# Kernel tuning notes

Hardware: AMD Instinct MI355X
Metric: run time of the kernel (lower is better)

The kernel has to match this reference:

```python
import jax, jax.numpy as jnp
import numpy as np

T, N, XD, H, Z, E = 6, 4096, 64, 256, 128, 131072


def setup_inputs() -> dict:
    key = jax.random.key(0)
    ks = jax.random.split(key, 16)
    f32 = jnp.float32
    def rn(k, shp):
        return jax.random.normal(k, shp, f32)
    def gl(k, shp):  # glorot-ish init, scaled by fan_in
        return jax.random.normal(k, shp, f32) * np.float32(1.0 / np.sqrt(shp[-2]))
    return {
        "x": rn(ks[0], (T, N, XD)),
        "edges": jax.random.randint(ks[1], (T, 2, E), 0, N, dtype=jnp.int32),
        "eps": rn(ks[2], (T, N, Z)),
        "drop_u": jax.random.uniform(ks[3], (T, N, Z), f32),
        "phi_x_w": gl(ks[4], (XD, H)), "phi_x_b": jnp.zeros((H,), f32),
        "phi_z_w": gl(ks[5], (Z, H)), "phi_z_b": jnp.zeros((H,), f32),
        "enc_w": gl(ks[6], (2 * H, H)),
        "enc_mu_w": gl(ks[7], (H, Z)),
        "enc_lv_w": gl(ks[8], (H, Z)),
        "prior_w": gl(ks[9], (H, H)), "prior_b": jnp.zeros((H,), f32),
        "prior_mu_w": gl(ks[10], (H, Z)), "prior_mu_b": jnp.zeros((Z,), f32),
        "prior_lv_w": gl(ks[11], (H, Z)), "prior_lv_b": jnp.zeros((Z,), f32),
        "gru_wx": gl(ks[12], (4, 2 * H, H)),  # gates i,f,o,c; x-side GCN weights
        "gru_wh": gl(ks[13], (4, H, H)),      # gates i,f,o,c; h-side GCN weights
    }


def reference(x, edges, eps, drop_u, phi_x_w, phi_x_b, phi_z_w, phi_z_b,
              enc_w, enc_mu_w, enc_lv_w, prior_w, prior_b,
              prior_mu_w, prior_mu_b, prior_lv_w, prior_lv_b,
              gru_wx, gru_wh):
    T_, N_, _ = x.shape
    H_ = phi_x_w.shape[1]
    h = jnp.zeros((N_, H_), x.dtype)
    c = jnp.zeros((N_, H_), x.dtype)
    loop = jnp.arange(N_, dtype=edges.dtype)
    enc_mus, prior_mus = [], []
    dec_t = None
    for t in range(T_):  # fixed small T; edge structure differs per step
        row = jnp.concatenate([edges[t, 0], loop])  # add self loops
        col = jnp.concatenate([edges[t, 1], loop])
        deg = jax.ops.segment_sum(jnp.ones(row.shape, x.dtype), row, num_segments=N_)
        dinv = jnp.where(deg > 0, jax.lax.rsqrt(deg), jnp.zeros((), x.dtype))
        norm = (dinv[row] * dinv[col])[:, None]

        def gcn(xx, W):
            # GCNConv: xW, gather at col, scale by sym-norm, scatter-add at row
            return jax.ops.segment_sum(norm * (xx @ W)[col], row, num_segments=N_)

        phi_x_t = jax.nn.relu(x[t] @ phi_x_w + phi_x_b)
        enc_t = jax.nn.relu(gcn(jnp.concatenate([phi_x_t, h], axis=1), enc_w))
        enc_mu_t = gcn(enc_t, enc_mu_w)
        enc_std_t = jax.nn.softplus(gcn(enc_t, enc_lv_w))
        prior_t = jax.nn.relu(h @ prior_w + prior_b)
        prior_mu_t = prior_t @ prior_mu_w + prior_mu_b
        _prior_std_t = jax.nn.softplus(prior_t @ prior_lv_w + prior_lv_b)  # computed as in original, unused in returns
        z_t = eps[t] * enc_std_t + enc_mu_t  # original: eps.mul(logvar).add_(mu)
        phi_z_t = jax.nn.relu(z_t @ phi_z_w + phi_z_b)
        # InnerProductDecoder with dropout(p=0.5, training=True), identity act
        z_drop = jnp.where(drop_u[t] < 0.5, z_t * 2.0, jnp.zeros((), x.dtype))
        dec_t = z_drop @ z_drop.T  # [N, N]
        # graph-LSTM step (n_layer = 1)
        xin = jnp.concatenate([phi_x_t, phi_z_t], axis=1)  # [N, 2H]
        gi = jax.nn.sigmoid(gcn(xin, gru_wx[0]) + gcn(h, gru_wh[0]))
        gf = jax.nn.sigmoid(gcn(xin, gru_wx[1]) + gcn(h, gru_wh[1]))
        go = jax.nn.sigmoid(gcn(xin, gru_wx[2]) + gcn(h, gru_wh[2]))
        ct = jnp.tanh(gcn(xin, gru_wx[3]) + gcn(h, gru_wh[3]))
        c_new = gf * h + gi * ct    # faithful to original: F_g * h[i] (not c)
        h_new = go * jnp.tanh(c)    # faithful to original: uses old c[i]
        h, c = h_new, c_new
        enc_mus.append(enc_mu_t)
        prior_mus.append(prior_mu_t)
    return jnp.stack(enc_mus), jnp.stack(prior_mus), h[None], dec_t
```

## Files before the change

kernel.cpp:

```cpp
#include <hip/hip_runtime.h>
#include <hip/hip_bf16.h>
#include <math.h>

#define T_  6
#define NN  4096
#define XD_ 64
#define H_  256
#define ZZ  128
#define EE  131072

typedef unsigned short u16;
typedef __attribute__((ext_vector_type(8))) short short8;
typedef __attribute__((ext_vector_type(8))) unsigned short u16x8;
typedef __attribute__((ext_vector_type(4))) float f32x4;

__device__ __forceinline__ float bf2f(u16 u) { return __uint_as_float(((unsigned)u) << 16); }
__device__ __forceinline__ u16 f2bf(float f) {
    unsigned x = __float_as_uint(f);
    return (u16)((x + 0x7FFFu + ((x >> 16) & 1u)) >> 16);
}

__global__ void k_deg(const int* __restrict__ edges, int* __restrict__ degcnt) {
    int t = blockIdx.y;
    int e = blockIdx.x * 256 + threadIdx.x;
    const int* rows = edges + (size_t)t * 2 * EE;
    atomicAdd(&degcnt[t * NN + rows[e]], 1);
}

__global__ void k_scan_dinv(const int* __restrict__ degcnt_all,
                            int* __restrict__ row_start_all,
                            int* __restrict__ cursor_all,
                            float* __restrict__ dinv_all) {
    __shared__ int sbuf[1024];
    int tt = blockIdx.x;
    const int* degcnt = degcnt_all + tt * NN;
    int* row_start = row_start_all + tt * (NN + 1);
    int* cursor = cursor_all + tt * NN;
    float* dinv = dinv_all + tt * NN;
    int t = threadIdx.x;
    int b = t * 4;
    int v0 = degcnt[b + 0], v1 = degcnt[b + 1], v2 = degcnt[b + 2], v3 = degcnt[b + 3];
    dinv[b + 0] = rsqrtf((float)(v0 + 1));
    dinv[b + 1] = rsqrtf((float)(v1 + 1));
    dinv[b + 2] = rsqrtf((float)(v2 + 1));
    dinv[b + 3] = rsqrtf((float)(v3 + 1));
    int s = v0 + v1 + v2 + v3;
    sbuf[t] = s;
    __syncthreads();
    for (int off = 1; off < 1024; off <<= 1) {
        int x = sbuf[t];
        int y = (t >= off) ? sbuf[t - off] : 0;
        __syncthreads();
        sbuf[t] = x + y;
        __syncthreads();
    }
    int excl = sbuf[t] - s;
    int r0 = excl, r1 = excl + v0, r2 = r1 + v1, r3 = r2 + v2;
    row_start[b + 0] = r0; cursor[b + 0] = r0;
    row_start[b + 1] = r1; cursor[b + 1] = r1;
    row_start[b + 2] = r2; cursor[b + 2] = r2;
    row_start[b + 3] = r3; cursor[b + 3] = r3;
    if (t == 1023) row_start[NN] = r3 + v3;
}

__global__ void k_scatter(const int* __restrict__ edges,
                          int* __restrict__ cursor, const float* __restrict__ dinv,
                          int* __restrict__ col_idx, float* __restrict__ val) {
    int t = blockIdx.y;
    int e = blockIdx.x * 256 + threadIdx.x;
    const int* rows = edges + (size_t)t * 2 * EE;
    const int* cols = rows + EE;
    int r = rows[e], cc = cols[e];
    int pos = atomicAdd(&cursor[t * NN + r], 1);
    col_idx[(size_t)t * EE + pos] = cc;
    val[(size_t)t * EE + pos] = dinv[t * NN + r] * dinv[t * NN + cc];
}

__device__ __forceinline__ void sp_row_wave(const u16* __restrict__ Y,
                                            const int* __restrict__ row_start,
                                            const int* __restrict__ col_idx,
                                            const float* __restrict__ val,
                                            const float* __restrict__ dinv,
                                            u16* __restrict__ outp, int ldo, int r) {
    int lane = threadIdx.x & 63;
    int half = lane >> 5;
    int cg = lane & 31;
    int s0 = row_start[r], s1 = row_start[r + 1];
    float a[8] = {0.f, 0.f, 0.f, 0.f, 0.f, 0.f, 0.f, 0.f};
    for (int base = s0; base < s1; base += 64) {
        int n = s1 - base; if (n > 64) n = 64;
        int cl = 0; float vl = 0.f;
        if (base + lane < s1) { cl = col_idx[base + lane]; vl = val[base + lane]; }
        for (int e = 0; e < n; e += 2) {
            int ei = e + half;
            int cc = __shfl(cl, ei);
            float v = (ei < n) ? __shfl(vl, ei) : 0.f;
            u16x8 y = *(const u16x8*)(Y + (size_t)cc * H_ + cg * 8);
#pragma unroll
            for (int j = 0; j < 8; ++j) a[j] += v * bf2f(y[j]);
        }
    }
#pragma unroll
    for (int j = 0; j < 8; ++j) a[j] += __shfl_xor(a[j], 32);
    if (half == 0) {
        float dr = dinv[r], sc = dr * dr;
        u16x8 ys = *(const u16x8*)(Y + (size_t)r * H_ + cg * 8);
        u16x8 o;
#pragma unroll
        for (int j = 0; j < 8; ++j) o[j] = f2bf(a[j] + sc * bf2f(ys[j]));
        *(u16x8*)(outp + (size_t)r * ldo + cg * 8) = o;
    }
}

__global__ void k_spmm(const u16* __restrict__ Y1,
                       const int* __restrict__ row_start_all, const int* __restrict__ col_idx_all,
                       const float* __restrict__ val_all, const float* __restrict__ dinv_all,
                       u16* __restrict__ out1, int ldo,
                       long long sY, long long sO) {
    int t = blockIdx.y;
    int w = threadIdx.x >> 6;
    sp_row_wave(Y1 + (size_t)t * sY, row_start_all + (size_t)t * (NN + 1),
                col_idx_all + (size_t)t * EE, val_all + (size_t)t * EE,
                dinv_all + (size_t)t * NN, out1 + (size_t)t * sO, ldo,
                blockIdx.x * 4 + w);
}

template<int MF>
__device__ __forceinline__ void mm_core(const u16* __restrict__ A, int lda,
                                        const u16* __restrict__ BT, int ldbt, int K,
                                        int row0, int col0,
                                        f32x4 acc[MF][MF], char* smem) {
    constexpr int TILE = MF * 32;
    u16* As = (u16*)smem;
    u16* Bs = As + TILE * 64;
    const int lane = threadIdx.x & 63;
    const int w = threadIdx.x >> 6;
    const int wr = (w >> 1) * (TILE / 2);
    const int wc = (w & 1) * (TILE / 2);

    int gRow[MF], gCol[MF];
#pragma unroll
    for (int i = 0; i < MF; ++i) {
        int G = (w * MF + i) * 64 + lane;
        int r = G >> 3;
        gRow[i] = r;
        gCol[i] = ((G & 7) ^ (r & 7)) << 3;
    }

    for (int k0 = 0; k0 < K; k0 += 64) {
#pragma unroll
        for (int i = 0; i < MF; ++i) {
            const u16* sa = A + (size_t)(row0 + gRow[i]) * lda + k0 + gCol[i];
            __builtin_amdgcn_global_load_lds(
                (const __attribute__((address_space(1))) void*)sa,
                (__attribute__((address_space(3))) void*)(As + (w * MF + i) * 512), 16, 0, 0);
            const u16* sb = BT + (size_t)(col0 + gRow[i]) * ldbt + k0 + gCol[i];
            __builtin_amdgcn_global_load_lds(
                (const __attribute__((address_space(1))) void*)sb,
                (__attribute__((address_space(3))) void*)(Bs + (w * MF + i) * 512), 16, 0, 0);
        }
        __syncthreads();
#pragma unroll
        for (int kk = 0; kk < 2; ++kk) {
            short8 a[MF], b[MF];
#pragma unroll
            for (int mf = 0; mf < MF; ++mf) {
                int r = wr + mf * 16 + (lane & 15);
                int off = (r * 128 + kk * 64 + (lane >> 4) * 16) ^ ((r & 7) << 4);
                a[mf] = *(const short8*)((const char*)As + off);
            }
#pragma unroll
            for (int nf = 0; nf < MF; ++nf) {
                int r = wc + nf * 16 + (lane & 15);
                int off = (r * 128 + kk * 64 + (lane >> 4) * 16) ^ ((r & 7) << 4);
                b[nf] = *(const short8*)((const char*)Bs + off);
            }
#pragma unroll
            for (int mf = 0; mf < MF; ++mf)
#pragma unroll
                for (int nf = 0; nf < MF; ++nf)
                    acc[mf][nf] = __builtin_amdgcn_mfma_f32_16x16x32_bf16(
                        a[mf], b[nf], acc[mf][nf], 0, 0, 0);
        }
        __syncthreads();
    }
}

template<int MF>
__launch_bounds__(256)
__global__ void k_mm(const u16* __restrict__ A, int lda,
                     const u16* __restrict__ BT, int ldbt, int K,
                     float* __restrict__ C0, int ldc0,
                     u16* __restrict__ C1, int ldc1,
                     const float* __restrict__ bias, int act,
                     float* __restrict__ C2,
                     const float* __restrict__ du, u16* __restrict__ zdOut) {
    constexpr int TILE = MF * 32;
    constexpr int STAGE_B = TILE * 64 * 2 * 2;
    constexpr int EPI_B = (MF == 2) ? 64 * 68 * 4 : 0;
    constexpr int SMEM_B = STAGE_B > EPI_B ? STAGE_B : EPI_B;
    __shared__ alignas(16) char smem[SMEM_B];

    const int tid = threadIdx.x;
    const int lane = tid & 63;
    const int w = tid >> 6;
    const int row0 = blockIdx.y * TILE;
    const int col0 = blockIdx.x * TILE;
    const int wr = (w >> 1) * (TILE / 2);
    const int wc = (w & 1) * (TILE / 2);

    f32x4 acc[MF][MF];
#pragma unroll
    for (int i = 0; i < MF; ++i)
#pragma unroll
        for (int j = 0; j < MF; ++j)
            acc[i][j] = f32x4{0.f, 0.f, 0.f, 0.f};

    mm_core<MF>(A, lda, BT, ldbt, K, row0, col0, acc, smem);

    const int ci = lane & 15;
    const int ri = (lane >> 4) * 4;

    if constexpr (MF == 2) {
        if (act == 4) {
            float (*epi)[68] = (float(*)[68])smem;
#pragma unroll
            for (int mf = 0; mf < 2; ++mf)
#pragma unroll
                for (int nf = 0; nf < 2; ++nf)
#pragma unroll
                    for (int i = 0; i < 4; ++i)
                        epi[wr + mf * 16 + ri + i][wc + nf * 16 + ci] = acc[mf][nf][i];
            __syncthreads();
            float* muo = C0; const float* eps = C2; u16* zo = C1;
#pragma unroll
            for (int k = 0; k < 8; ++k) {
                int p = tid + k * 256;
                int row = p >> 5, jl = p & 31;
                float mu = epi[row][jl * 2];
                float sp = epi[row][jl * 2 + 1];
                float sd = (sp > 20.f) ? sp : log1pf(expf(sp));
                int idx = (row0 + row) * ZZ + (col0 >> 1) + jl;
                muo[idx] = mu;
                u16 z16 = f2bf(eps[idx] * sd + mu);
                zo[idx] = z16;
                if (zdOut)
                    zdOut[idx] = (du[idx] < 0.5f) ? f2bf(2.f * bf2f(z16)) : (u16)0;
            }
            return;
        }
    }

#pragma unroll
    for (int mf = 0; mf < MF; ++mf) {
#pragma unroll
        for (int nf = 0; nf < MF; ++nf) {
            int row = row0 + wr + mf * 16 + ri;
            int col = col0 + wc + nf * 16 + ci;
            if (C1) {
                float bv = bias ? bias[col] : 0.f;
#pragma unroll
                for (int i = 0; i < 4; ++i) {
                    float v = acc[mf][nf][i] + bv;
                    if (act == 1) v = fmaxf(v, 0.f);
                    C1[(size_t)(row + i) * ldc1 + col] = f2bf(v);
                }
            } else {
                float bv = bias ? bias[col] : 0.f;
#pragma unroll
                for (int i = 0; i < 4; ++i)
                    C0[(size_t)(row + i) * ldc0 + col] = acc[mf][nf][i] + bv;
            }
        }
    }
}

__launch_bounds__(256)
__global__ void k_dual(const u16* __restrict__ A0, int lda0, const u16* __restrict__ BT0,
                       int ldbt0, int K0, u16* __restrict__ Cb0, int ldcb0,
                       const u16* __restrict__ A1, int lda1, const u16* __restrict__ BT1,
                       int ldbt1, int K1, float* __restrict__ Cf1, int ldcf1,
                       const float* __restrict__ bias1) {
    __shared__ alignas(16) char smem[16384];
    const int z = blockIdx.z;
    if (z && blockIdx.x >= 2) return;
    const u16* A = z ? A1 : A0;   int lda = z ? lda1 : lda0;
    const u16* BT = z ? BT1 : BT0; int ldbt = z ? ldbt1 : ldbt0;
    int K = z ? K1 : K0;

    const int lane = threadIdx.x & 63;
    const int w = threadIdx.x >> 6;
    const int row0 = blockIdx.y * 64;
    const int col0 = blockIdx.x * 64;
    const int wr = (w >> 1) * 32, wc = (w & 1) * 32;

    f32x4 acc[2][2];
#pragma unroll
    for (int i = 0; i < 2; ++i)
#pragma unroll
        for (int j = 0; j < 2; ++j) acc[i][j] = f32x4{0.f, 0.f, 0.f, 0.f};
    mm_core<2>(A, lda, BT, ldbt, K, row0, col0, acc, smem);

    const int ci = lane & 15, ri = (lane >> 4) * 4;
#pragma unroll
    for (int mf = 0; mf < 2; ++mf)
#pragma unroll
        for (int nf = 0; nf < 2; ++nf) {
            int row = row0 + wr + mf * 16 + ri;
            int col = col0 + wc + nf * 16 + ci;
            if (z == 0) {
#pragma unroll
                for (int i = 0; i < 4; ++i)
                    Cb0[(size_t)(row + i) * ldcb0 + col] = f2bf(fmaxf(acc[mf][nf][i], 0.f));
            } else {
                float bv = bias1[col];
#pragma unroll
                for (int i = 0; i < 4; ++i)
                    Cf1[(size_t)(row + i) * ldcf1 + col] = acc[mf][nf][i] + bv;
            }
        }
}

__launch_bounds__(256)
__global__ void k_sp_mm(const u16* __restrict__ Y, const int* __restrict__ row_start,
                        const int* __restrict__ col_idx, const float* __restrict__ val,
                        const float* __restrict__ dinv, u16* __restrict__ spOut, int spLdo,
                        int doSp,
                        const u16* __restrict__ A, int lda, const u16* __restrict__ BT,
                        int ldbt, int K, float* __restrict__ Cf, int ldcf,
                        u16* __restrict__ Cb, int ldcb,
                        const float* __restrict__ bias, int gx) {
    __shared__ alignas(16) char smem[16384];
    int bid = blockIdx.x;
    if (bid < NN / 4) {
        if (!doSp) return;
        int w = threadIdx.x >> 6;
        sp_row_wave(Y, row_start, col_idx, val, dinv, spOut, spLdo, bid * 4 + w);
        return;
    }
    int b2 = bid - NN / 4;
    const int row0 = (b2 / gx) * 64;
    const int col0 = (b2 % gx) * 64;
    const int lane = threadIdx.x & 63;
    const int w = threadIdx.x >> 6;
    const int wr = (w >> 1) * 32, wc = (w & 1) * 32;
    f32x4 acc[2][2];
#pragma unroll
    for (int i = 0; i < 2; ++i)
#pragma unroll
        for (int j = 0; j < 2; ++j) acc[i][j] = f32x4{0.f, 0.f, 0.f, 0.f};
    mm_core<2>(A, lda, BT, ldbt, K, row0, col0, acc, smem);
    const int ci = lane & 15, ri = (lane >> 4) * 4;
#pragma unroll
    for (int mf = 0; mf < 2; ++mf)
#pragma unroll
        for (int nf = 0; nf < 2; ++nf) {
            int row = row0 + wr + mf * 16 + ri;
            int col = col0 + wc + nf * 16 + ci;
            float bv = bias ? bias[col] : 0.f;
            if (Cb) {
#pragma unroll
                for (int i = 0; i < 4; ++i)
                    Cb[(size_t)(row + i) * ldcb + col] = f2bf(fmaxf(acc[mf][nf][i] + bv, 0.f));
            } else {
#pragma unroll
                for (int i = 0; i < 4; ++i)
                    Cf[(size_t)(row + i) * ldcf + col] = acc[mf][nf][i] + bv;
            }
        }
}

__launch_bounds__(256)
__global__ void k_gates(const u16* __restrict__ XIN, const u16* __restrict__ BgT,
                        float* __restrict__ h, float* __restrict__ c,
                        u16* __restrict__ hbf, float* __restrict__ hOut,
                        int skipSH) {
    __shared__ alignas(16) char smem[128 * 68 * 4];
    u16* As = (u16*)smem;
    u16* Bs = As + 128 * 64;
    const int tid = threadIdx.x;
    const int lane = tid & 63;
    const int w = tid >> 6;
    const int row0 = blockIdx.y * 128;
    const int col0 = blockIdx.x * 64;
    const int wrB = (w >> 1) * 64;
    const int wc = (w & 1) * 32;

    f32x4 acc[4][2];
#pragma unroll
    for (int i = 0; i < 4; ++i)
#pragma unroll
        for (int j = 0; j < 2; ++j) acc[i][j] = f32x4{0.f, 0.f, 0.f, 0.f};

    int aRow[4], aCol[4];
#pragma unroll
    for (int i = 0; i < 4; ++i) {
        int G = (w * 4 + i) * 64 + lane;
        int r = G >> 3;
        aRow[i] = r;
        aCol[i] = ((G & 7) ^ (r & 7)) << 3;
    }
    int bRow[2], bCol[2];
#pragma unroll
    for (int i = 0; i < 2; ++i) {
        int G = (w * 2 + i) * 64 + lane;
        int r = G >> 3;
        bRow[i] = r;
        bCol[i] = ((G & 7) ^ (r & 7)) << 3;
    }

    const int nIter = skipSH ? 8 : 12;
    for (int it = 0; it < nIter; ++it) {
        int k0 = it * 64 + ((skipSH && it >= 4) ? 256 : 0);
#pragma unroll
        for (int i = 0; i < 4; ++i) {
            const u16* sa = XIN + (size_t)(row0 + aRow[i]) * 768 + k0 + aCol[i];
            __builtin_amdgcn_global_load_lds(
                (const __attribute__((address_space(1))) void*)sa,
                (__attribute__((address_space(3))) void*)(As + (w * 4 + i) * 512), 16, 0, 0);
        }
#pragma unroll
        for (int i = 0; i < 2; ++i) {
            const u16* sb = BgT + (size_t)(col0 + bRow[i]) * 768 + k0 + bCol[i];
            __builtin_amdgcn_global_load_lds(
                (const __attribute__((address_space(1))) void*)sb,
                (__attribute__((address_space(3))) void*)(Bs + (w * 2 + i) * 512), 16, 0, 0);
        }
        __syncthreads();
#pragma unroll
        for (int kk = 0; kk < 2; ++kk) {
            short8 a[4], b[2];
#pragma unroll
            for (int mf = 0; mf < 4; ++mf) {
                int r = wrB + mf * 16 + (lane & 15);
                int off = (r * 128 + kk * 64 + (lane >> 4) * 16) ^ ((r & 7) << 4);
                a[mf] = *(const short8*)((const char*)As + off);
            }
#pragma unroll
            for (int nf = 0; nf < 2; ++nf) {
                int r = wc + nf * 16 + (lane & 15);
                int off = (r * 128 + kk * 64 + (lane >> 4) * 16) ^ ((r & 7) << 4);
                b[nf] = *(const short8*)((const char*)Bs + off);
            }
#pragma unroll
            for (int mf = 0; mf < 4; ++mf)
#pragma unroll
                for (int nf = 0; nf < 2; ++nf)
                    acc[mf][nf] = __builtin_amdgcn_mfma_f32_16x16x32_bf16(
                        a[mf], b[nf], acc[mf][nf], 0, 0, 0);
        }
        __syncthreads();
    }

    const int ci = lane & 15;
    const int ri = (lane >> 4) * 4;
    float (*epi)[68] = (float(*)[68])smem;
#pragma unroll
    for (int mf = 0; mf < 4; ++mf)
#pragma unroll
        for (int nf = 0; nf < 2; ++nf)
#pragma unroll
            for (int i = 0; i < 4; ++i)
                epi[wrB + mf * 16 + ri + i][wc + nf * 16 + ci] = acc[mf][nf][i];
    __syncthreads();
#pragma unroll
    for (int k = 0; k < 8; ++k) {
        int p = tid + k * 256;
        int row = p >> 4, jl = p & 15;
        float4 g4 = *(const float4*)&epi[row][jl * 4];
        float gi = 1.f / (1.f + expf(-g4.x));
        float gf = 1.f / (1.f + expf(-g4.y));
        float go = 1.f / (1.f + expf(-g4.z));
        float ct = tanhf(g4.w);
        int idx = (row0 + row) * H_ + (col0 >> 2) + jl;
        float ho = h[idx], co = c[idx];
        float cn = gf * ho + gi * ct;
        float hn = go * tanhf(co);
        h[idx] = hn;
        c[idx] = cn;
        hbf[idx] = f2bf(hn);
        if (hOut) hOut[idx] = hn;
    }
}

__global__ void k_cvt(const float* __restrict__ in, u16* __restrict__ outp, int n4) {
    int i = blockIdx.x * 256 + threadIdx.x;
    if (i >= n4) return;
    float4 v = ((const float4*)in)[i];
    ((ushort4*)outp)[i] = make_ushort4(f2bf(v.x), f2bf(v.y), f2bf(v.z), f2bf(v.w));
}

__global__ void k_prep(const float* __restrict__ phi_x_w, const float* __restrict__ phi_z_w,
                       const float* __restrict__ enc_w, const float* __restrict__ prior_w,
                       const float* __restrict__ prior_mu_w,
                       const float* __restrict__ enc_mu_w, const float* __restrict__ enc_lv_w,
                       const float* __restrict__ gru_wx, const float* __restrict__ gru_wh,
                       u16* __restrict__ phi_x_wT, u16* __restrict__ phi_z_wT,
                       u16* __restrict__ enc_wT, u16* __restrict__ prior_wT,
                       u16* __restrict__ prior_mu_wT, u16* __restrict__ mulvT,
                       u16* __restrict__ BgT) {
    int idx = blockIdx.x * 256 + threadIdx.x;
    if (idx < 16384) {
        int j = idx >> 6, k = idx & 63;
        phi_x_wT[idx] = f2bf(phi_x_w[k * 256 + j]);
        return;
    }
    idx -= 16384;
    if (idx < 32768) {
        int j = idx >> 7, k = idx & 127;
        phi_z_wT[idx] = f2bf(phi_z_w[k * 256 + j]);
        return;
    }
    idx -= 32768;
    if (idx < 131072) {
        int j = idx >> 9, k = idx & 511;
        enc_wT[idx] = f2bf(enc_w[k * 256 + j]);
        return;
    }
    idx -= 131072;
    if (idx < 65536) {
        int j = idx >> 8, k = idx & 255;
        prior_wT[idx] = f2bf(prior_w[k * 256 + j]);
        return;
    }
    idx -= 65536;
    if (idx < 32768) {
        int j = idx >> 8, k = idx & 255;
        prior_mu_wT[idx] = f2bf(prior_mu_w[k * 128 + j]);
        return;
    }
    idx -= 32768;
    if (idx < 65536) {
        int cp = idx >> 8, k = idx & 255;
        int j = cp >> 1, s = cp & 1;
        float v = s ? enc_lv_w[k * 128 + j] : enc_mu_w[k * 128 + j];
        mulvT[idx] = f2bf(v);
        return;
    }
    idx -= 65536;
    if (idx < 786432) {
        int cp = idx / 768, k = idx % 768;
        int g = cp & 3, j = cp >> 2;
        float v;
        if (k < 256)      v = gru_wx[((size_t)g * 512 + k) * 256 + j];
        else if (k < 512) v = gru_wh[((size_t)g * 256 + (k - 256)) * 256 + j];
        else              v = gru_wx[((size_t)g * 512 + (k - 256)) * 256 + j];
        BgT[idx] = f2bf(v);
    }
}

extern "C" void kernel_launch(void* const* d_in, const int* in_sizes, int n_in,
                              void* d_out_v, int out_size, void* d_ws, size_t ws_size,
                              hipStream_t stream) {
    (void)in_sizes; (void)n_in; (void)out_size;
    const float* x          = (const float*)d_in[0];
    const int*   edges      = (const int*)d_in[1];
    const float* eps        = (const float*)d_in[2];
    const float* drop_u     = (const float*)d_in[3];
    const float* phi_x_w    = (const float*)d_in[4];
    const float* phi_x_b    = (const float*)d_in[5];
    const float* phi_z_w    = (const float*)d_in[6];
    const float* phi_z_b    = (const float*)d_in[7];
    const float* enc_w      = (const float*)d_in[8];
    const float* enc_mu_w   = (const float*)d_in[9];
    const float* enc_lv_w   = (const float*)d_in[10];
    const float* prior_w    = (const float*)d_in[11];
    const float* prior_b    = (const float*)d_in[12];
    const float* prior_mu_w = (const float*)d_in[13];
    const float* prior_mu_b = (const float*)d_in[14];
    const float* gru_wx     = (const float*)d_in[17];
    const float* gru_wh     = (const float*)d_in[18];
    float* out = (float*)d_out_v;

    char* base = (char*)d_ws;
    size_t cur = 0;
    auto carve = [&](size_t bytes) -> void* {
        void* p = base + cur;
        cur += (bytes + 255) & ~(size_t)255;
        return p;
    };
    float* h         = (float*)carve((size_t)NN * H_ * 4);
    float* c         = (float*)carve((size_t)NN * H_ * 4);
    u16* h_bf        = (u16*)carve((size_t)NN * H_ * 2);
    size_t hcz_bytes = cur;
    float* dinv      = (float*)carve((size_t)T_ * NN * 4);
    int*   degcnt    = (int*)carve((size_t)T_ * NN * 4);
    int*   row_start = (int*)carve((size_t)T_ * (NN + 1) * 4);
    int*   cursor    = (int*)carve((size_t)T_ * NN * 4);
    int*   col_idx   = (int*)carve((size_t)T_ * EE * 4);
    float* val       = (float*)carve((size_t)T_ * EE * 4);
    u16* x_bf        = (u16*)carve((size_t)T_ * NN * XD_ * 2);
    u16* phi6        = (u16*)carve((size_t)T_ * NN * H_ * 2);
    u16* phi         = (u16*)carve((size_t)NN * H_ * 2);
    u16* enc_t       = (u16*)carve((size_t)NN * H_ * 2);
    u16* SEb         = (u16*)carve((size_t)NN * H_ * 2);
    u16* prior_t     = (u16*)carve((size_t)NN * H_ * 2);
    u16* XIN6        = (u16*)carve((size_t)T_ * NN * 768 * 2);
    u16* zbuf        = (u16*)carve((size_t)NN * ZZ * 2);
    u16* zd          = (u16*)carve((size_t)NN * ZZ * 2);
    u16* phi_x_wT    = (u16*)carve((size_t)XD_ * H_ * 2);
    u16* phi_z_wT    = (u16*)carve((size_t)ZZ * H_ * 2);
    u16* enc_wT      = (u16*)carve((size_t)512 * H_ * 2);
    u16* prior_wT    = (u16*)carve((size_t)H_ * H_ * 2);
    u16* prior_mu_wT = (u16*)carve((size_t)ZZ * H_ * 2);
    u16* mulvT       = (u16*)carve((size_t)H_ * H_ * 2);
    u16* BgT         = (u16*)carve((size_t)1024 * 768 * 2);
    if (cur > ws_size) return;

    const size_t NZ = (size_t)NN * ZZ;
    const size_t HOFF = (size_t)2 * T_ * NZ;
    const size_t DECOFF = HOFF + (size_t)NN * H_;

    k_cvt<<<(T_ * NN * XD_ / 4 + 255) / 256, 256, 0, stream>>>(x, x_bf, T_ * NN * XD_ / 4);
    k_prep<<<(1130496 + 255) / 256, 256, 0, stream>>>(
        phi_x_w, phi_z_w, enc_w, prior_w, prior_mu_w, enc_mu_w, enc_lv_w,
        gru_wx, gru_wh,
        phi_x_wT, phi_z_wT, enc_wT, prior_wT, prior_mu_wT, mulvT, BgT);

    hipMemsetAsync(degcnt, 0, (size_t)T_ * NN * 4, stream);
    k_deg<<<dim3(EE / 256, T_), 256, 0, stream>>>(edges, degcnt);
    k_scan_dinv<<<T_, 1024, 0, stream>>>(degcnt, row_start, cursor, dinv);
    k_scatter<<<dim3(EE / 256, T_), 256, 0, stream>>>(edges, cursor, dinv, col_idx, val);

    k_mm<2><<<dim3(4, (T_ * NN) / 64), 256, 0, stream>>>(x_bf, XD_, phi_x_wT, XD_, XD_,
        nullptr, 0, phi6, H_, phi_x_b, 1, nullptr, nullptr, nullptr);
    k_spmm<<<dim3(NN / 4, T_), 256, 0, stream>>>(phi6, row_start, col_idx, val, dinv,
        XIN6, 768, (long long)NN * H_, (long long)NN * 768);

    hipMemsetAsync(h, 0, hcz_bytes, stream);

    for (int t = 0; t < T_; ++t) {
        const int* rs_t = row_start + (size_t)t * (NN + 1);
        const int* ci_t = col_idx + (size_t)t * EE;
        const float* vv_t = val + (size_t)t * EE;
        const float* dv_t = dinv + (size_t)t * NN;
        u16* xin_t = XIN6 + (size_t)t * NN * 768;
        int last = (t == T_ - 1);

        k_sp_mm<<<NN / 4 + 256, 256, 0, stream>>>(h_bf, rs_t, ci_t, vv_t, dv_t,
            xin_t + 256, 768, t > 0,
            h_bf, H_, prior_wT, H_, H_, nullptr, 0, prior_t, H_, prior_b, 4);
        k_dual<<<dim3(4, 64, 2), 256, 0, stream>>>(
            xin_t, 768, enc_wT, 512, (t == 0) ? 256 : 512, enc_t, H_,
            prior_t, H_, prior_mu_wT, H_, H_,
            out + (size_t)(T_ + t) * NZ, ZZ, prior_mu_b);
        k_spmm<<<dim3(NN / 4, 1), 256, 0, stream>>>(enc_t, rs_t, ci_t, vv_t, dv_t,
                                                    SEb, H_, 0, 0);
        k_mm<2><<<dim3(4, 64), 256, 0, stream>>>(SEb, H_, mulvT, H_, H_,
            out + (size_t)t * NZ, 0, zbuf, 0, nullptr, 4, (float*)(eps + (size_t)t * NZ),
            last ? drop_u + (size_t)t * NZ : nullptr, last ? zd : nullptr);
        k_mm<2><<<dim3(4, 64), 256, 0, stream>>>(zbuf, ZZ, phi_z_wT, ZZ, ZZ,
            nullptr, 0, phi, H_, phi_z_b, 1, nullptr, nullptr, nullptr);
        k_spmm<<<dim3(NN / 4, 1), 256, 0, stream>>>(phi, rs_t, ci_t, vv_t, dv_t,
                                                    xin_t + 512, 768, 0, 0);
        k_gates<<<dim3(16, 32), 256, 0, stream>>>(xin_t, BgT, h, c, h_bf,
            last ? out + HOFF : nullptr, t == 0);
    }

    k_mm<4><<<dim3(32, 32), 256, 0, stream>>>(zd, ZZ, zd, ZZ, ZZ,
        out + DECOFF, NN, nullptr, 0, nullptr, 0, nullptr, nullptr, nullptr);
}
```

Measured before the change: 611.1 us.

## Fuse latent head, reparameterisation and phi_z matmul into one kernel

```diff
diff --git a/kernel.cpp b/kernel.cpp
--- a/kernel.cpp
+++ b/kernel.cpp
@@ -1,5 +1,4 @@
 #include <hip/hip_runtime.h>
-#include <hip/hip_bf16.h>
 #include <math.h>
 
 #define T_  6
@@ -84,31 +83,37 @@
                                             u16* __restrict__ outp, int ldo, int r) {
     int lane = threadIdx.x & 63;
     int half = lane >> 5;
-    int cg = lane & 31;
+    int cg2 = lane & 31;
     int s0 = row_start[r], s1 = row_start[r + 1];
     float a[8] = {0.f, 0.f, 0.f, 0.f, 0.f, 0.f, 0.f, 0.f};
     for (int base = s0; base < s1; base += 64) {
         int n = s1 - base; if (n > 64) n = 64;
         int cl = 0; float vl = 0.f;
         if (base + lane < s1) { cl = col_idx[base + lane]; vl = val[base + lane]; }
-        for (int e = 0; e < n; e += 2) {
+        for (int e = 0; e < n; e += 4) {
             int ei = e + half;
-            int cc = __shfl(cl, ei);
-            float v = (ei < n) ? __shfl(vl, ei) : 0.f;
-            u16x8 y = *(const u16x8*)(Y + (size_t)cc * H_ + cg * 8);
-#pragma unroll
-            for (int j = 0; j < 8; ++j) a[j] += v * bf2f(y[j]);
+            int ej = e + 2 + half;
+            int cc0 = __shfl(cl, ei);
+            float v0 = (ei < n) ? __shfl(vl, ei) : 0.f;
+            int cc1 = __shfl(cl, ej);
+            float v1 = (ej < n) ? __shfl(vl, ej) : 0.f;
+            u16x8 y0 = *(const u16x8*)(Y + (size_t)cc0 * H_ + cg2 * 8);
+            u16x8 y1 = *(const u16x8*)(Y + (size_t)cc1 * H_ + cg2 * 8);
+#pragma unroll
+            for (int j = 0; j < 8; ++j) a[j] += v0 * bf2f(y0[j]);
+#pragma unroll
+            for (int j = 0; j < 8; ++j) a[j] += v1 * bf2f(y1[j]);
         }
     }
 #pragma unroll
     for (int j = 0; j < 8; ++j) a[j] += __shfl_xor(a[j], 32);
     if (half == 0) {
         float dr = dinv[r], sc = dr * dr;
-        u16x8 ys = *(const u16x8*)(Y + (size_t)r * H_ + cg * 8);
+        u16x8 ys = *(const u16x8*)(Y + (size_t)r * H_ + cg2 * 8);
         u16x8 o;
 #pragma unroll
         for (int j = 0; j < 8; ++j) o[j] = f2bf(a[j] + sc * bf2f(ys[j]));
-        *(u16x8*)(outp + (size_t)r * ldo + cg * 8) = o;
+        *(u16x8*)(outp + (size_t)r * ldo + cg2 * 8) = o;
     }
 }
 
@@ -186,24 +191,63 @@
     }
 }
 
+__device__ __forceinline__ void zacc2(f32x4 acc[2][2]) {
+#pragma unroll
+    for (int i = 0; i < 2; ++i)
+#pragma unroll
+        for (int j = 0; j < 2; ++j) acc[i][j] = f32x4{0.f, 0.f, 0.f, 0.f};
+}
+
+__device__ __forceinline__ void epi_bf16relu(f32x4 acc[2][2], u16* __restrict__ C,
+                                             int ldc, int row0, int col0,
+                                             const float* __restrict__ bias) {
+    const int lane = threadIdx.x & 63, w = threadIdx.x >> 6;
+    const int wr = (w >> 1) * 32, wc = (w & 1) * 32;
+    const int ci = lane & 15, ri = (lane >> 4) * 4;
+#pragma unroll
+    for (int mf = 0; mf < 2; ++mf)
+#pragma unroll
+        for (int nf = 0; nf < 2; ++nf) {
+            int row = row0 + wr + mf * 16 + ri;
+            int col = col0 + wc + nf * 16 + ci;
+            float bv = bias ? bias[col] : 0.f;
+#pragma unroll
+            for (int i = 0; i < 4; ++i)
+                C[(size_t)(row + i) * ldc + col] = f2bf(fmaxf(acc[mf][nf][i] + bv, 0.f));
+        }
+}
+
+__device__ __forceinline__ void epi_f32b(f32x4 acc[2][2], float* __restrict__ C,
+                                         int ldc, int row0, int col0,
+                                         const float* __restrict__ bias) {
+    const int lane = threadIdx.x & 63, w = threadIdx.x >> 6;
+    const int wr = (w >> 1) * 32, wc = (w & 1) * 32;
+    const int ci = lane & 15, ri = (lane >> 4) * 4;
+#pragma unroll
+    for (int mf = 0; mf < 2; ++mf)
+#pragma unroll
+        for (int nf = 0; nf < 2; ++nf) {
+            int row = row0 + wr + mf * 16 + ri;
+            int col = col0 + wc + nf * 16 + ci;
+            float bv = bias[col];
+#pragma unroll
+            for (int i = 0; i < 4; ++i)
+                C[(size_t)(row + i) * ldc + col] = acc[mf][nf][i] + bv;
+        }
+}
+
 template<int MF>
 __launch_bounds__(256)
 __global__ void k_mm(const u16* __restrict__ A, int lda,
                      const u16* __restrict__ BT, int ldbt, int K,
                      float* __restrict__ C0, int ldc0,
                      u16* __restrict__ C1, int ldc1,
-                     const float* __restrict__ bias, int act,
-                     float* __restrict__ C2,
-                     const float* __restrict__ du, u16* __restrict__ zdOut) {
+                     const float* __restrict__ bias, int act) {
     constexpr int TILE = MF * 32;
-    constexpr int STAGE_B = TILE * 64 * 2 * 2;
-    constexpr int EPI_B = (MF == 2) ? 64 * 68 * 4 : 0;
-    constexpr int SMEM_B = STAGE_B > EPI_B ? STAGE_B : EPI_B;
-    __shared__ alignas(16) char smem[SMEM_B];
-
-    const int tid = threadIdx.x;
-    const int lane = tid & 63;
-    const int w = tid >> 6;
+    __shared__ alignas(16) char smem[TILE * 64 * 4];
+
+    const int lane = threadIdx.x & 63;
+    const int w = threadIdx.x >> 6;
     const int row0 = blockIdx.y * TILE;
     const int col0 = blockIdx.x * TILE;
     const int wr = (w >> 1) * (TILE / 2);
@@ -220,37 +264,6 @@
 
     const int ci = lane & 15;
     const int ri = (lane >> 4) * 4;
-
-    if constexpr (MF == 2) {
-        if (act == 4) {
-            float (*epi)[68] = (float(*)[68])smem;
-#pragma unroll
-            for (int mf = 0; mf < 2; ++mf)
-#pragma unroll
-                for (int nf = 0; nf < 2; ++nf)
-#pragma unroll
-                    for (int i = 0; i < 4; ++i)
-                        epi[wr + mf * 16 + ri + i][wc + nf * 16 + ci] = acc[mf][nf][i];
-            __syncthreads();
-            float* muo = C0; const float* eps = C2; u16* zo = C1;
-#pragma unroll
-            for (int k = 0; k < 8; ++k) {
-                int p = tid + k * 256;
-                int row = p >> 5, jl = p & 31;
-                float mu = epi[row][jl * 2];
-                float sp = epi[row][jl * 2 + 1];
-                float sd = (sp > 20.f) ? sp : log1pf(expf(sp));
-                int idx = (row0 + row) * ZZ + (col0 >> 1) + jl;
-                muo[idx] = mu;
-                u16 z16 = f2bf(eps[idx] * sd + mu);
-                zo[idx] = z16;
-                if (zdOut)
-                    zdOut[idx] = (du[idx] < 0.5f) ? f2bf(2.f * bf2f(z16)) : (u16)0;
-            }
-            return;
-        }
-    }
-
 #pragma unroll
     for (int mf = 0; mf < MF; ++mf) {
 #pragma unroll
@@ -287,38 +300,12 @@
     const u16* A = z ? A1 : A0;   int lda = z ? lda1 : lda0;
     const u16* BT = z ? BT1 : BT0; int ldbt = z ? ldbt1 : ldbt0;
     int K = z ? K1 : K0;
-
-    const int lane = threadIdx.x & 63;
-    const int w = threadIdx.x >> 6;
     const int row0 = blockIdx.y * 64;
     const int col0 = blockIdx.x * 64;
-    const int wr = (w >> 1) * 32, wc = (w & 1) * 32;
-
-    f32x4 acc[2][2];
-#pragma unroll
-    for (int i = 0; i < 2; ++i)
-#pragma unroll
-        for (int j = 0; j < 2; ++j) acc[i][j] = f32x4{0.f, 0.f, 0.f, 0.f};
+    f32x4 acc[2][2]; zacc2(acc);
     mm_core<2>(A, lda, BT, ldbt, K, row0, col0, acc, smem);
-
-    const int ci = lane & 15, ri = (lane >> 4) * 4;
-#pragma unroll
-    for (int mf = 0; mf < 2; ++mf)
-#pragma unroll
-        for (int nf = 0; nf < 2; ++nf) {
-            int row = row0 + wr + mf * 16 + ri;
-            int col = col0 + wc + nf * 16 + ci;
-            if (z == 0) {
-#pragma unroll
-                for (int i = 0; i < 4; ++i)
-                    Cb0[(size_t)(row + i) * ldcb0 + col] = f2bf(fmaxf(acc[mf][nf][i], 0.f));
-            } else {
-                float bv = bias1[col];
-#pragma unroll
-                for (int i = 0; i < 4; ++i)
-                    Cf1[(size_t)(row + i) * ldcf1 + col] = acc[mf][nf][i] + bv;
-            }
-        }
+    if (z == 0) epi_bf16relu(acc, Cb0, ldcb0, row0, col0, nullptr);
+    else        epi_f32b(acc, Cf1, ldcf1, row0, col0, bias1);
 }
 
 __launch_bounds__(256)
@@ -327,8 +314,7 @@
                         const float* __restrict__ dinv, u16* __restrict__ spOut, int spLdo,
                         int doSp,
                         const u16* __restrict__ A, int lda, const u16* __restrict__ BT,
-                        int ldbt, int K, float* __restrict__ Cf, int ldcf,
-                        u16* __restrict__ Cb, int ldcb,
+                        int ldbt, int K, u16* __restrict__ Cb, int ldcb,
                         const float* __restrict__ bias, int gx) {
     __shared__ alignas(16) char smem[16384];
     int bid = blockIdx.x;
@@ -341,33 +327,150 @@
     int b2 = bid - NN / 4;
     const int row0 = (b2 / gx) * 64;
     const int col0 = (b2 % gx) * 64;
-    const int lane = threadIdx.x & 63;
-    const int w = threadIdx.x >> 6;
-    const int wr = (w >> 1) * 32, wc = (w & 1) * 32;
-    f32x4 acc[2][2];
-#pragma unroll
-    for (int i = 0; i < 2; ++i)
-#pragma unroll
-        for (int j = 0; j < 2; ++j) acc[i][j] = f32x4{0.f, 0.f, 0.f, 0.f};
+    f32x4 acc[2][2]; zacc2(acc);
     mm_core<2>(A, lda, BT, ldbt, K, row0, col0, acc, smem);
-    const int ci = lane & 15, ri = (lane >> 4) * 4;
-#pragma unroll
-    for (int mf = 0; mf < 2; ++mf)
-#pragma unroll
-        for (int nf = 0; nf < 2; ++nf) {
-            int row = row0 + wr + mf * 16 + ri;
-            int col = col0 + wc + nf * 16 + ci;
-            float bv = bias ? bias[col] : 0.f;
-            if (Cb) {
-#pragma unroll
-                for (int i = 0; i < 4; ++i)
-                    Cb[(size_t)(row + i) * ldcb + col] = f2bf(fmaxf(acc[mf][nf][i] + bv, 0.f));
-            } else {
-#pragma unroll
-                for (int i = 0; i < 4; ++i)
-                    Cf[(size_t)(row + i) * ldcf + col] = acc[mf][nf][i] + bv;
-            }
-        }
+    epi_bf16relu(acc, Cb, ldcb, row0, col0, bias);
+}
+
+__launch_bounds__(256)
+__global__ void k_p45(const u16* __restrict__ SEb, const u16* __restrict__ mulvT,
+                      float* __restrict__ out_mu, const float* __restrict__ eps_t,
+                      const float* __restrict__ du_t, u16* __restrict__ zdOut,
+                      const u16* __restrict__ pzwT, const float* __restrict__ pz_b,
+                      u16* __restrict__ phi) {
+    __shared__ alignas(16) char smem[40960];
+    u16* As  = (u16*)smem;
+    u16* Bm  = As + 4096;
+    u16* Bs2 = Bm + 4096;
+    char* zl = (char*)(Bs2 + 4096);
+
+    const int tid = threadIdx.x;
+    const int lane = tid & 63;
+    const int w = tid >> 6;
+    const int row0 = blockIdx.x * 64;
+    const int wr = (w >> 1) * 32;
+    const int wc = (w & 1) * 32;
+    const int ci = lane & 15;
+    const int ri = (lane >> 4) * 4;
+
+    int gRow[2], gCol[2];
+#pragma unroll
+    for (int i = 0; i < 2; ++i) {
+        int G = (w * 2 + i) * 64 + lane;
+        int r = G >> 3;
+        gRow[i] = r;
+        gCol[i] = ((G & 7) ^ (r & 7)) << 3;
+    }
+
+    for (int p = 0; p < 2; ++p) {
+        f32x4 amu[2][2], asp[2][2];
+        zacc2(amu); zacc2(asp);
+        for (int k0 = 0; k0 < 256; k0 += 64) {
+#pragma unroll
+            for (int i = 0; i < 2; ++i) {
+                const u16* sa = SEb + (size_t)(row0 + gRow[i]) * 256 + k0 + gCol[i];
+                __builtin_amdgcn_global_load_lds(
+                    (const __attribute__((address_space(1))) void*)sa,
+                    (__attribute__((address_space(3))) void*)(As + (w * 2 + i) * 512), 16, 0, 0);
+                const u16* sm = mulvT + (size_t)(p * 64 + gRow[i]) * 256 + k0 + gCol[i];
+                __builtin_amdgcn_global_load_lds(
+                    (const __attribute__((address_space(1))) void*)sm,
+                    (__attribute__((address_space(3))) void*)(Bm + (w * 2 + i) * 512), 16, 0, 0);
+                const u16* ss = mulvT + (size_t)(128 + p * 64 + gRow[i]) * 256 + k0 + gCol[i];
+                __builtin_amdgcn_global_load_lds(
+                    (const __attribute__((address_space(1))) void*)ss,
+                    (__attribute__((address_space(3))) void*)(Bs2 + (w * 2 + i) * 512), 16, 0, 0);
+            }
+            __syncthreads();
+#pragma unroll
+            for (int kk = 0; kk < 2; ++kk) {
+                short8 a[2], bm[2], bs[2];
+#pragma unroll
+                for (int mf = 0; mf < 2; ++mf) {
+                    int r = wr + mf * 16 + (lane & 15);
+                    int off = (r * 128 + kk * 64 + (lane >> 4) * 16) ^ ((r & 7) << 4);
+                    a[mf] = *(const short8*)((const char*)As + off);
+                }
+#pragma unroll
+                for (int nf = 0; nf < 2; ++nf) {
+                    int r = wc + nf * 16 + (lane & 15);
+                    int off = (r * 128 + kk * 64 + (lane >> 4) * 16) ^ ((r & 7) << 4);
+                    bm[nf] = *(const short8*)((const char*)Bm + off);
+                    bs[nf] = *(const short8*)((const char*)Bs2 + off);
+                }
+#pragma unroll
+                for (int mf = 0; mf < 2; ++mf)
+#pragma unroll
+                    for (int nf = 0; nf < 2; ++nf) {
+                        amu[mf][nf] = __builtin_amdgcn_mfma_f32_16x16x32_bf16(
+                            a[mf], bm[nf], amu[mf][nf], 0, 0, 0);
+                        asp[mf][nf] = __builtin_amdgcn_mfma_f32_16x16x32_bf16(
+                            a[mf], bs[nf], asp[mf][nf], 0, 0, 0);
+                    }
+            }
+            __syncthreads();
+        }
+#pragma unroll
+        for (int mf = 0; mf < 2; ++mf)
+#pragma unroll
+            for (int nf = 0; nf < 2; ++nf)
+#pragma unroll
+                for (int i = 0; i < 4; ++i) {
+                    int row_l = wr + mf * 16 + ri + i;
+                    int col_l = wc + nf * 16 + ci;
+                    int j = p * 64 + col_l;
+                    size_t gidx = (size_t)(row0 + row_l) * ZZ + j;
+                    float mu = amu[mf][nf][i];
+                    out_mu[gidx] = mu;
+                    float sp = asp[mf][nf][i];
+                    float sd = (sp > 20.f) ? sp : log1pf(expf(sp));
+                    u16 z16 = f2bf(eps_t[gidx] * sd + mu);
+                    int zb = p * 8192 + ((row_l * 128 + col_l * 2) ^ ((row_l & 7) << 4));
+                    *(u16*)(zl + zb) = z16;
+                    if (zdOut)
+                        zdOut[gidx] = (du_t[gidx] < 0.5f) ? f2bf(2.f * bf2f(z16)) : (u16)0;
+                }
+    }
+    __syncthreads();
+
+    for (int oc = 0; oc < 4; ++oc) {
+        f32x4 acc[2][2]; zacc2(acc);
+        for (int k0 = 0; k0 < 128; k0 += 64) {
+#pragma unroll
+            for (int i = 0; i < 2; ++i) {
+                const u16* sb = pzwT + (size_t)(oc * 64 + gRow[i]) * 128 + k0 + gCol[i];
+                __builtin_amdgcn_global_load_lds(
+                    (const __attribute__((address_space(1))) void*)sb,
+                    (__attribute__((address_space(3))) void*)(Bm + (w * 2 + i) * 512), 16, 0, 0);
+            }
+            __syncthreads();
+#pragma unroll
+            for (int kk = 0; kk < 2; ++kk) {
+                short8 a[2], b[2];
+#pragma unroll
+                for (int mf = 0; mf < 2; ++mf) {
+                    int r = wr + mf * 16 + (lane & 15);
+                    int off = (k0 >> 6) * 8192 +
+                              ((r * 128 + kk * 64 + (lane >> 4) * 16) ^ ((r & 7) << 4));
+                    a[mf] = *(const short8*)(zl + off);
+                }
+#pragma unroll
+                for (int nf = 0; nf < 2; ++nf) {
+                    int r = wc + nf * 16 + (lane & 15);
+                    int off = (r * 128 + kk * 64 + (lane >> 4) * 16) ^ ((r & 7) << 4);
+                    b[nf] = *(const short8*)((const char*)Bm + off);
+                }
+#pragma unroll
+                for (int mf = 0; mf < 2; ++mf)
+#pragma unroll
+                    for (int nf = 0; nf < 2; ++nf)
+                        acc[mf][nf] = __builtin_amdgcn_mfma_f32_16x16x32_bf16(
+                            a[mf], b[nf], acc[mf][nf], 0, 0, 0);
+            }
+            __syncthreads();
+        }
+        epi_bf16relu(acc, phi, H_, row0, oc * 64, pz_b);
+    }
 }
 
 __launch_bounds__(256)
@@ -375,7 +478,7 @@
                         float* __restrict__ h, float* __restrict__ c,
                         u16* __restrict__ hbf, float* __restrict__ hOut,
                         int skipSH) {
-    __shared__ alignas(16) char smem[128 * 68 * 4];
+    __shared__ alignas(16) char smem[34816];
     u16* As = (u16*)smem;
     u16* Bs = As + 128 * 64;
     const int tid = threadIdx.x;
@@ -483,13 +586,6 @@
     }
 }
 
-__global__ void k_cvt(const float* __restrict__ in, u16* __restrict__ outp, int n4) {
-    int i = blockIdx.x * 256 + threadIdx.x;
-    if (i >= n4) return;
-    float4 v = ((const float4*)in)[i];
-    ((ushort4*)outp)[i] = make_ushort4(f2bf(v.x), f2bf(v.y), f2bf(v.z), f2bf(v.w));
-}
-
 __global__ void k_prep(const float* __restrict__ phi_x_w, const float* __restrict__ phi_z_w,
                        const float* __restrict__ enc_w, const float* __restrict__ prior_w,
                        const float* __restrict__ prior_mu_w,
@@ -498,7 +594,9 @@
                        u16* __restrict__ phi_x_wT, u16* __restrict__ phi_z_wT,
                        u16* __restrict__ enc_wT, u16* __restrict__ prior_wT,
                        u16* __restrict__ prior_mu_wT, u16* __restrict__ mulvT,
-                       u16* __restrict__ BgT) {
+                       u16* __restrict__ BgT,
+                       const float* __restrict__ x, u16* __restrict__ x_bf,
+                       int* __restrict__ degcnt) {
     int idx = blockIdx.x * 256 + threadIdx.x;
     if (idx < 16384) {
         int j = idx >> 6, k = idx & 63;
@@ -532,8 +630,7 @@
     idx -= 32768;
     if (idx < 65536) {
         int cp = idx >> 8, k = idx & 255;
-        int j = cp >> 1, s = cp & 1;
-        float v = s ? enc_lv_w[k * 128 + j] : enc_mu_w[k * 128 + j];
+        float v = (cp < 128) ? enc_mu_w[k * 128 + cp] : enc_lv_w[k * 128 + (cp - 128)];
         mulvT[idx] = f2bf(v);
         return;
     }
@@ -546,7 +643,17 @@
         else if (k < 512) v = gru_wh[((size_t)g * 256 + (k - 256)) * 256 + j];
         else              v = gru_wx[((size_t)g * 512 + (k - 256)) * 256 + j];
         BgT[idx] = f2bf(v);
-    }
+        return;
+    }
+    idx -= 786432;
+    if (idx < 393216) {
+        float4 v = ((const float4*)x)[idx];
+        ((ushort4*)x_bf)[idx] = make_ushort4(f2bf(v.x), f2bf(v.y), f2bf(v.z), f2bf(v.w));
+        return;
+    }
+    idx -= 393216;
+    if (idx < 6144)
+        ((int4*)degcnt)[idx] = make_int4(0, 0, 0, 0);
 }
 
 extern "C" void kernel_launch(void* const* d_in, const int* in_sizes, int n_in,
@@ -591,12 +698,11 @@
     float* val       = (float*)carve((size_t)T_ * EE * 4);
     u16* x_bf        = (u16*)carve((size_t)T_ * NN * XD_ * 2);
     u16* phi6        = (u16*)carve((size_t)T_ * NN * H_ * 2);
-    u16* phi         = (u16*)carve((size_t)NN * H_ * 2);
+    u16* phiz        = (u16*)carve((size_t)NN * H_ * 2);
     u16* enc_t       = (u16*)carve((size_t)NN * H_ * 2);
     u16* SEb         = (u16*)carve((size_t)NN * H_ * 2);
     u16* prior_t     = (u16*)carve((size_t)NN * H_ * 2);
     u16* XIN6        = (u16*)carve((size_t)T_ * NN * 768 * 2);
-    u16* zbuf        = (u16*)carve((size_t)NN * ZZ * 2);
     u16* zd          = (u16*)carve((size_t)NN * ZZ * 2);
     u16* phi_x_wT    = (u16*)carve((size_t)XD_ * H_ * 2);
     u16* phi_z_wT    = (u16*)carve((size_t)ZZ * H_ * 2);
@@ -611,22 +717,18 @@
     const size_t HOFF = (size_t)2 * T_ * NZ;
     const size_t DECOFF = HOFF + (size_t)NN * H_;
 
-    k_cvt<<<(T_ * NN * XD_ / 4 + 255) / 256, 256, 0, stream>>>(x, x_bf, T_ * NN * XD_ / 4);
-    k_prep<<<(1130496 + 255) / 256, 256, 0, stream>>>(
+    k_prep<<<(1529856 + 255) / 256, 256, 0, stream>>>(
         phi_x_w, phi_z_w, enc_w, prior_w, prior_mu_w, enc_mu_w, enc_lv_w,
         gru_wx, gru_wh,
-        phi_x_wT, phi_z_wT, enc_wT, prior_wT, prior_mu_wT, mulvT, BgT);
-
-    hipMemsetAsync(degcnt, 0, (size_t)T_ * NN * 4, stream);
+        phi_x_wT, phi_z_wT, enc_wT, prior_wT, prior_mu_wT, mulvT, BgT,
+        x, x_bf, degcnt);
     k_deg<<<dim3(EE / 256, T_), 256, 0, stream>>>(edges, degcnt);
     k_scan_dinv<<<T_, 1024, 0, stream>>>(degcnt, row_start, cursor, dinv);
     k_scatter<<<dim3(EE / 256, T_), 256, 0, stream>>>(edges, cursor, dinv, col_idx, val);
-
     k_mm<2><<<dim3(4, (T_ * NN) / 64), 256, 0, stream>>>(x_bf, XD_, phi_x_wT, XD_, XD_,
-        nullptr, 0, phi6, H_, phi_x_b, 1, nullptr, nullptr, nullptr);
+        nullptr, 0, phi6, H_, phi_x_b, 1);
     k_spmm<<<dim3(NN / 4, T_), 256, 0, stream>>>(phi6, row_start, col_idx, val, dinv,
         XIN6, 768, (long long)NN * H_, (long long)NN * 768);
-
     hipMemsetAsync(h, 0, hcz_bytes, stream);
 
     for (int t = 0; t < T_; ++t) {
@@ -639,24 +741,23 @@
 
         k_sp_mm<<<NN / 4 + 256, 256, 0, stream>>>(h_bf, rs_t, ci_t, vv_t, dv_t,
             xin_t + 256, 768, t > 0,
-            h_bf, H_, prior_wT, H_, H_, nullptr, 0, prior_t, H_, prior_b, 4);
+            h_bf, H_, prior_wT, H_, H_, prior_t, H_, prior_b, 4);
         k_dual<<<dim3(4, 64, 2), 256, 0, stream>>>(
             xin_t, 768, enc_wT, 512, (t == 0) ? 256 : 512, enc_t, H_,
             prior_t, H_, prior_mu_wT, H_, H_,
             out + (size_t)(T_ + t) * NZ, ZZ, prior_mu_b);
         k_spmm<<<dim3(NN / 4, 1), 256, 0, stream>>>(enc_t, rs_t, ci_t, vv_t, dv_t,
                                                     SEb, H_, 0, 0);
-        k_mm<2><<<dim3(4, 64), 256, 0, stream>>>(SEb, H_, mulvT, H_, H_,
-            out + (size_t)t * NZ, 0, zbuf, 0, nullptr, 4, (float*)(eps + (size_t)t * NZ),
-            last ? drop_u + (size_t)t * NZ : nullptr, last ? zd : nullptr);
-        k_mm<2><<<dim3(4, 64), 256, 0, stream>>>(zbuf, ZZ, phi_z_wT, ZZ, ZZ,
-            nullptr, 0, phi, H_, phi_z_b, 1, nullptr, nullptr, nullptr);
-        k_spmm<<<dim3(NN / 4, 1), 256, 0, stream>>>(phi, rs_t, ci_t, vv_t, dv_t,
+        k_p45<<<64, 256, 0, stream>>>(SEb, mulvT, out + (size_t)t * NZ,
+            eps + (size_t)t * NZ,
+            last ? drop_u + (size_t)t * NZ : nullptr, last ? zd : nullptr,
+            phi_z_wT, phi_z_b, phiz);
+        k_spmm<<<dim3(NN / 4, 1), 256, 0, stream>>>(phiz, rs_t, ci_t, vv_t, dv_t,
                                                     xin_t + 512, 768, 0, 0);
         k_gates<<<dim3(16, 32), 256, 0, stream>>>(xin_t, BgT, h, c, h_bf,
             last ? out + HOFF : nullptr, t == 0);
     }
 
     k_mm<4><<<dim3(32, 32), 256, 0, stream>>>(zd, ZZ, zd, ZZ, ZZ,
-        out + DECOFF, NN, nullptr, 0, nullptr, 0, nullptr, nullptr, nullptr);
-}
+        out + DECOFF, NN, nullptr, 0, nullptr, 0);
+}
```

Result: slower. 740.4 us (+21.2%).
